# Kernel optimization log

Measured on AMD Instinct MI355X. Metric: run time of the kernel, lower is better.

## Reference

```python
import jax, jax.numpy as jnp
import numpy as np

LEAKY_SLOPE = 0.2

def setup_inputs() -> dict:
    key = jax.random.key(0)
    k1, k2, k3, k4, k5 = jax.random.split(key, 5)
    N, F_IN, H, D = 8192, 256, 4, 64
    x = jax.random.normal(k1, (N, F_IN), dtype=jnp.float32)
    adj = jax.random.randint(k2, (N, N), 0, 2, dtype=jnp.int32)
    W = jax.random.normal(k3, (F_IN, H * D), dtype=jnp.float32) * 0.05
    a_l = jax.random.normal(k4, (H, D), dtype=jnp.float32) * 0.05
    a_r = jax.random.normal(k5, (H, D), dtype=jnp.float32) * 0.05
    return {"x": x, "adj": adj, "W": W, "a_l": a_l, "a_r": a_r}

def reference(x, adj, W, a_l, a_r):
    N = x.shape[0]
    H, D = a_l.shape
    # projected node features: (N, H, D)
    h = (x @ W).reshape(N, H, D)
    score_l = jnp.einsum('nhd,hd->nh', h, a_l)  # (N, H)
    score_r = jnp.einsum('nhd,hd->nh', h, a_r)  # (N, H)
    # logits[i, j, h] = score_l[i, h] + score_r[j, h]
    logits = score_l[:, None, :] + score_r[None, :, :]
    logits = jax.nn.leaky_relu(logits, negative_slope=LEAKY_SLOPE)
    # mask: keep edge (i,j) if adj[i,j] + eye[i,j] != 0
    keep = (adj + jnp.eye(N, dtype=adj.dtype)) != 0  # (N, N)
    logits = jnp.where(keep[:, :, None], logits, -jnp.inf)
    # softmax over neighbors j (axis=1), matching torch softmax(dim=1)
    attn = jax.nn.softmax(logits, axis=1)  # (N, N, H)
    out = jnp.einsum('ijh,jhf->ihf', attn, h)  # (N, H, D)
    return out.reshape(N, H * D)  # concat=True
```

## Files before the change

### kernel.cpp

```cpp
#include <hip/hip_runtime.h>
#include <hip/hip_bf16.h>
#include <hip/hip_fp16.h>

#define N 8192
#define FIN 256
#define HD 256
#define LEAKY 0.2f

typedef short sh8 __attribute__((ext_vector_type(8)));
typedef _Float16 h8 __attribute__((ext_vector_type(8)));
typedef _Float16 h2 __attribute__((ext_vector_type(2)));
typedef float f32x4 __attribute__((ext_vector_type(4)));
typedef int   i32x4 __attribute__((ext_vector_type(4)));

__device__ __forceinline__ int pack2bf(float a, float b){
  __hip_bfloat162 t = __float22bfloat162_rn(make_float2(a, b));
  union { __hip_bfloat162 h; int i; } u;
  u.h = t;
  return u.i;
}

__device__ __forceinline__ h2 u2h2(unsigned u){ union{unsigned u; h2 h;} c; c.u=u; return c.h; }
__device__ __forceinline__ unsigned h22u(h2 h){ union{unsigned u; h2 h;} c; c.h=h; return c.u; }

__global__ void k_wt(const float* __restrict__ W, __hip_bfloat16* __restrict__ Wt){
  __shared__ float t[16][17];
  int tx = threadIdx.x, ty = threadIdx.y;
  int bx = blockIdx.x*16, by = blockIdx.y*16;
  t[ty][tx] = W[(by+ty)*HD + (bx+tx)];
  __syncthreads();
  Wt[(bx+ty)*FIN + (by+tx)] = __float2bfloat16(t[tx][ty]);
}

__global__ __launch_bounds__(256) void k_pack(const int* __restrict__ adj,
                                              unsigned* __restrict__ bits){
  const int g = blockIdx.x*256 + threadIdx.x;
  const i32x4 a = *(const i32x4*)(adj + (size_t)g*4);
  const int sub = g & 7;
  unsigned wpart = 0;
  #pragma unroll
  for (int e = 0; e < 4; ++e){
    const int jj = sub*4 + e;
    wpart |= ((unsigned)a[e] & 1u) << ((jj >> 1) + ((jj & 1) << 4));
  }
  wpart |= __shfl_xor(wpart, 1);
  wpart |= __shfl_xor(wpart, 2);
  wpart |= __shfl_xor(wpart, 4);
  if (sub == 0){
    const int t = g >> 3;
    const int i = t >> 8;
    const int c = t & 255;
    if ((i >> 5) == c){
      const int k = i & 31;
      wpart |= 1u << ((k >> 1) + ((k & 1) << 4));
    }
    bits[t] = wpart;
  }
}

__global__ __launch_bounds__(256, 2) void k_h(
    const float* __restrict__ x, const __hip_bfloat16* __restrict__ Wt,
    const float* __restrict__ a_l, const float* __restrict__ a_r,
    _Float16* __restrict__ ht, float* __restrict__ El, float* __restrict__ El2,
    _Float16* __restrict__ Erh, _Float16* __restrict__ Er2h)
{
  const int lane = threadIdx.x & 63;
  const int w = threadIdx.x >> 6;
  const int r0 = lane & 15, q = lane >> 4;
  const int c0 = w*64;
  const int n0 = blockIdx.x*16;

  f32x4 acc[4];
  #pragma unroll
  for (int m = 0; m < 4; ++m) acc[m] = (f32x4){0.f, 0.f, 0.f, 0.f};

  for (int kb = 0; kb < 8; ++kb){
    const int k = kb*32 + q*8;
    sh8 af[4];
    #pragma unroll
    for (int m = 0; m < 4; ++m)
      af[m] = *(const sh8*)(Wt + (c0 + m*16 + r0)*FIN + k);
    const float* xp = x + (n0 + r0)*FIN + k;
    f32x4 xl = *(const f32x4*)xp;
    f32x4 xh = *(const f32x4*)(xp + 4);
    union { sh8 s; int i[4]; } bx;
    bx.i[0] = pack2bf(xl[0], xl[1]);
    bx.i[1] = pack2bf(xl[2], xl[3]);
    bx.i[2] = pack2bf(xh[0], xh[1]);
    bx.i[3] = pack2bf(xh[2], xh[3]);
    #pragma unroll
    for (int m = 0; m < 4; ++m)
      acc[m] = __builtin_amdgcn_mfma_f32_16x16x32_bf16(af[m], bx.s, acc[m], 0, 0, 0);
  }

  float pl = 0.f, pr = 0.f;
  #pragma unroll
  for (int m = 0; m < 4; ++m){
    #pragma unroll
    for (int reg = 0; reg < 4; ++reg){
      const int c = c0 + m*16 + q*4 + reg;
      const float v = acc[m][reg];
      ht[(size_t)c*N + (n0 + r0)] = (_Float16)v;
      pl += v*a_l[c];
      pr += v*a_r[c];
    }
  }
  pl += __shfl_xor(pl, 16); pl += __shfl_xor(pl, 32);
  pr += __shfl_xor(pr, 16); pr += __shfl_xor(pr, 32);
  if (lane < 16){
    const int n = n0 + r0;
    El  [w*N + n] = __expf(pl);
    El2 [w*N + n] = __expf(LEAKY*pl);
    Erh [w*N + n] = (_Float16)__expf(pr);
    Er2h[w*N + n] = (_Float16)__expf(LEAKY*pr);
  }
}

__global__ __launch_bounds__(256, 4) void k_attn(
    const unsigned* __restrict__ bits, const _Float16* __restrict__ ht,
    const float* __restrict__ El, const float* __restrict__ El2,
    const _Float16* __restrict__ Erh, const _Float16* __restrict__ Er2h,
    float* __restrict__ part, float* __restrict__ zpart)
{
  __shared__ __align__(16) char smem[40960];
  const int b = blockIdx.x;
  const int h = b >> 8, jq = (b >> 6) & 3, i128 = b & 63;
  const int tid = threadIdx.x;
  const int lane = tid & 63;
  const int w = tid >> 6;
  const int r0 = lane & 15, q = lane >> 4;
  const int ib = i128*128 + w*32;
  const int jbase = jq * 2048;

  const _Float16* gp = ht + (size_t)(h*64 + w*16 + (lane >> 2))*N
                          + jbase + (((lane & 3) ^ ((lane >> 3) & 3))*8);
  char* lb = smem + w*1024;
  const char* frp = smem + r0*64 + ((q ^ ((r0 >> 1) & 3)) << 4);

  {
    const _Float16* s1 = Erh  + h*N + jbase + w*512 + lane*8;
    const _Float16* s2 = Er2h + h*N + jbase + w*512 + lane*8;
    __builtin_amdgcn_global_load_lds(
      (const __attribute__((address_space(1))) void*)s1,
      (__attribute__((address_space(3))) void*)(smem + 32768 + w*1024), 16, 0, 0);
    __builtin_amdgcn_global_load_lds(
      (const __attribute__((address_space(1))) void*)s2,
      (__attribute__((address_space(3))) void*)(smem + 36864 + w*1024), 16, 0, 0);
  }
  const char* erp1 = smem + 32768 + q*16;
  const char* erp2 = smem + 36864 + q*16;

  const float* el_ = El  + h*N + ib + r0;
  const float* el2_= El2 + h*N + ib + r0;
  h2 elh[2], el2h[2];
  #pragma unroll
  for (int m = 0; m < 2; ++m){
    _Float16 a = (_Float16)el_[m*16];
    _Float16 c = (_Float16)el2_[m*16];
    elh[m]  = (h2){a, a};
    el2h[m] = (h2){c, c};
  }

  const unsigned* bp0 = bits + (size_t)(ib + r0)*(N/32) + jq*64;
  const unsigned* bp1 = bp0 + 16*(N/32);
  const int qs = q*4;

  union { h8 s; int i[4]; } onef;
  {
    int v = (r0 == 0) ? 0x3C003C00 : 0;
    onef.i[0]=v; onef.i[1]=v; onef.i[2]=v; onef.i[3]=v;
  }

  f32x4 acc[2][4];
  f32x4 accz[2];
  #pragma unroll
  for (int m = 0; m < 2; ++m){
    accz[m] = (f32x4){0.f,0.f,0.f,0.f};
    #pragma unroll
    for (int d = 0; d < 4; ++d)
      acc[m][d] = (f32x4){0.f,0.f,0.f,0.f};
  }

#define STAGE(bufoff, t) do { \
    const _Float16* _g = gp + (t)*128; \
    _Pragma("unroll") \
    for (int _s = 0; _s < 4; ++_s) \
      __builtin_amdgcn_global_load_lds( \
        (const __attribute__((address_space(1))) void*)(_g + _s*32), \
        (__attribute__((address_space(3))) void*)(lb + (bufoff) + _s*4096), 16, 0, 0); \
  } while(0)

  i32x4 bcur[2], bnxt[2];
  bcur[0] = *(const i32x4*)(bp0);
  bcur[1] = *(const i32x4*)(bp1);
  STAGE(0, 0);
  __syncthreads();

  for (int t = 0; t < 16; ++t){
    const int bo = (t & 1) ? 16384 : 0;
    const int bn = bo ^ 16384;
    const int tn = (t + 1) & 15;
    STAGE(bn, tn);
    bnxt[0] = *(const i32x4*)(bp0 + tn*4);
    bnxt[1] = *(const i32x4*)(bp1 + tn*4);

    #pragma unroll
    for (int ss = 0; ss < 4; ++ss){
      i32x4 er4  = *(const i32x4*)(erp1 + t*256 + ss*64);
      i32x4 er24 = *(const i32x4*)(erp2 + t*256 + ss*64);

      h8 hf[4];
      #pragma unroll
      for (int d = 0; d < 4; ++d)
        hf[d] = *(const h8*)(frp + bo + ss*4096 + d*1024);

      #pragma unroll
      for (int m = 0; m < 2; ++m){
        const unsigned wq = ((unsigned)bcur[m][ss]) >> qs;
        unsigned fu[4];
        #pragma unroll
        for (int p = 0; p < 4; ++p){
          const unsigned t32 = (wq >> p) & 0x10001u;
          const unsigned msk = t32 * 0xFFFFu;
          h2 w2 = __builtin_elementwise_max(elh[m]  * u2h2((unsigned)er4[p]),
                                            el2h[m] * u2h2((unsigned)er24[p]));
          fu[p] = h22u(w2) & msk;
        }
        union { h8 s; unsigned u[4]; } fa;
        fa.u[0]=fu[0]; fa.u[1]=fu[1]; fa.u[2]=fu[2]; fa.u[3]=fu[3];
        #pragma unroll
        for (int d = 0; d < 4; ++d)
          acc[m][d] = __builtin_amdgcn_mfma_f32_16x16x32_f16(fa.s, hf[d], acc[m][d], 0, 0, 0);
        accz[m] = __builtin_amdgcn_mfma_f32_16x16x32_f16(fa.s, onef.s, accz[m], 0, 0, 0);
      }
    }

    bcur[0] = bnxt[0]; bcur[1] = bnxt[1];
    __syncthreads();
  }

  if (r0 == 0){
    #pragma unroll
    for (int m = 0; m < 2; ++m)
      #pragma unroll
      for (int reg = 0; reg < 4; ++reg)
        zpart[(jq*4 + h)*N + ib + m*16 + q*4 + reg] = accz[m][reg];
  }

  float* pp = part + (size_t)jq*N*HD + h*64 + r0;
  #pragma unroll
  for (int m = 0; m < 2; ++m)
    #pragma unroll
    for (int d = 0; d < 4; ++d)
      #pragma unroll
      for (int reg = 0; reg < 4; ++reg)
        pp[(size_t)(ib + m*16 + q*4 + reg)*HD + d*16] = acc[m][d][reg];
#undef STAGE
}

__global__ void k_out(const float* __restrict__ part, const float* __restrict__ zpart,
                      float* __restrict__ out)
{
  const int t4 = (blockIdx.x*256 + threadIdx.x) * 4;
  const int i = t4 >> 8;
  const int h = (t4 & 255) >> 6;
  f32x4 a = *(const f32x4*)(part + t4);
  f32x4 bq = *(const f32x4*)(part + (size_t)N*HD + t4);
  f32x4 c = *(const f32x4*)(part + 2*(size_t)N*HD + t4);
  f32x4 d = *(const f32x4*)(part + 3*(size_t)N*HD + t4);
  float zz = zpart[h*N + i] + zpart[(4 + h)*N + i] + zpart[(8 + h)*N + i] + zpart[(12 + h)*N + i];
  f32x4 s = (a + bq + c + d) / zz;
  *(f32x4*)(out + t4) = s;
}

extern "C" void kernel_launch(void* const* d_in, const int* in_sizes, int n_in,
                              void* d_out, int out_size, void* d_ws, size_t ws_size,
                              hipStream_t stream) {
  const float* x   = (const float*)d_in[0];
  const int*   adj = (const int*)d_in[1];
  const float* W   = (const float*)d_in[2];
  const float* a_l = (const float*)d_in[3];
  const float* a_r = (const float*)d_in[4];
  float* out = (float*)d_out;

  char* ws = (char*)d_ws;
  __hip_bfloat16* Wt = (__hip_bfloat16*)ws;
  _Float16* ht   = (_Float16*)(ws + 131072);
  float*    El   = (float*)   (ws + 4325376);
  float*    El2  = (float*)   (ws + 4456448);
  _Float16* Erh  = (_Float16*)(ws + 4587520);
  _Float16* Er2h = (_Float16*)(ws + 4653056);
  float*    part = (float*)   (ws + 4718592);
  float*    zpart= (float*)   (ws + 38273024);
  unsigned* bits = (unsigned*)(ws + 38797312);

  k_wt  <<<dim3(16,16), dim3(16,16), 0, stream>>>(W, Wt);
  k_pack<<<N*N/4/256, 256, 0, stream>>>(adj, bits);
  k_h   <<<512, 256, 0, stream>>>(x, Wt, a_l, a_r, ht, El, El2, Erh, Er2h);
  k_attn<<<1024, 256, 0, stream>>>(bits, ht, El, El2, Erh, Er2h, part, zpart);
  k_out <<<N*HD/1024, 256, 0, stream>>>(part, zpart, out);
}
```

Baseline: 429.4 us.

## Split attention j-range into eighths with triple-buffered LDS staging

The attention kernel now splits the neighbour dimension into 8 chunks of 1024 instead of 4 of 2048, doubling the grid to 2048 blocks. Each tile is half as large, and LDS use drops so occupancy can rise to 5 blocks per SM. The staging moves from a double buffer with __syncthreads to a three-slot ring with explicit vmcnt waits and raw barriers, keeping two tiles in flight, and MFMA sections get raised wave priority. The cost is twice as many partial-sum buffers, which k_out must read and reduce, adding global memory traffic.

```diff
diff --git a/kernel.cpp b/kernel.cpp
--- a/kernel.cpp
+++ b/kernel.cpp
@@ -12,6 +12,7 @@
 typedef _Float16 h2 __attribute__((ext_vector_type(2)));
 typedef float f32x4 __attribute__((ext_vector_type(4)));
 typedef int   i32x4 __attribute__((ext_vector_type(4)));
+typedef int   i32x2 __attribute__((ext_vector_type(2)));
 
 __device__ __forceinline__ int pack2bf(float a, float b){
   __hip_bfloat162 t = __float22bfloat162_rn(make_float2(a, b));
@@ -116,21 +117,21 @@
   }
 }
 
-__global__ __launch_bounds__(256, 4) void k_attn(
+__global__ __launch_bounds__(256, 5) void k_attn(
     const unsigned* __restrict__ bits, const _Float16* __restrict__ ht,
     const float* __restrict__ El, const float* __restrict__ El2,
     const _Float16* __restrict__ Erh, const _Float16* __restrict__ Er2h,
     float* __restrict__ part, float* __restrict__ zpart)
 {
-  __shared__ __align__(16) char smem[40960];
+  __shared__ __align__(16) char smem[28672];
   const int b = blockIdx.x;
-  const int h = b >> 8, jq = (b >> 6) & 3, i128 = b & 63;
+  const int h = b >> 9, jq = (b >> 6) & 7, i128 = b & 63;
   const int tid = threadIdx.x;
   const int lane = tid & 63;
   const int w = tid >> 6;
   const int r0 = lane & 15, q = lane >> 4;
   const int ib = i128*128 + w*32;
-  const int jbase = jq * 2048;
+  const int jbase = jq * 1024;
 
   const _Float16* gp = ht + (size_t)(h*64 + w*16 + (lane >> 2))*N
                           + jbase + (((lane & 3) ^ ((lane >> 3) & 3))*8);
@@ -138,17 +139,15 @@
   const char* frp = smem + r0*64 + ((q ^ ((r0 >> 1) & 3)) << 4);
 
   {
-    const _Float16* s1 = Erh  + h*N + jbase + w*512 + lane*8;
-    const _Float16* s2 = Er2h + h*N + jbase + w*512 + lane*8;
+    const int arr = w >> 1, half = w & 1;
+    const _Float16* src = (arr ? Er2h : Erh) + h*N + jbase + half*512 + lane*8;
     __builtin_amdgcn_global_load_lds(
-      (const __attribute__((address_space(1))) void*)s1,
-      (__attribute__((address_space(3))) void*)(smem + 32768 + w*1024), 16, 0, 0);
-    __builtin_amdgcn_global_load_lds(
-      (const __attribute__((address_space(1))) void*)s2,
-      (__attribute__((address_space(3))) void*)(smem + 36864 + w*1024), 16, 0, 0);
-  }
-  const char* erp1 = smem + 32768 + q*16;
-  const char* erp2 = smem + 36864 + q*16;
+      (const __attribute__((address_space(1))) void*)src,
+      (__attribute__((address_space(3))) void*)(smem + 24576 + arr*2048 + half*1024 + lane*16),
+      16, 0, 0);
+  }
+  const char* erp1 = smem + 24576 + q*16;
+  const char* erp2 = smem + 26624 + q*16;
 
   const float* el_ = El  + h*N + ib + r0;
   const float* el2_= El2 + h*N + ib + r0;
@@ -161,7 +160,7 @@
     el2h[m] = (h2){c, c};
   }
 
-  const unsigned* bp0 = bits + (size_t)(ib + r0)*(N/32) + jq*64;
+  const unsigned* bp0 = bits + (size_t)(ib + r0)*(N/32) + jq*32;
   const unsigned* bp1 = bp0 + 16*(N/32);
   const int qs = q*4;
 
@@ -182,41 +181,43 @@
   }
 
 #define STAGE(bufoff, t) do { \
-    const _Float16* _g = gp + (t)*128; \
+    const _Float16* _g = gp + (t)*64; \
     _Pragma("unroll") \
-    for (int _s = 0; _s < 4; ++_s) \
+    for (int _s = 0; _s < 2; ++_s) \
       __builtin_amdgcn_global_load_lds( \
         (const __attribute__((address_space(1))) void*)(_g + _s*32), \
         (__attribute__((address_space(3))) void*)(lb + (bufoff) + _s*4096), 16, 0, 0); \
   } while(0)
 
-  i32x4 bcur[2], bnxt[2];
-  bcur[0] = *(const i32x4*)(bp0);
-  bcur[1] = *(const i32x4*)(bp1);
+  i32x2 bc0, bc1, bn0, bn1;
+  bc0 = *(const i32x2*)(bp0);
+  bc1 = *(const i32x2*)(bp1);
   STAGE(0, 0);
-  __syncthreads();
-
+  STAGE(8192, 1);
+  asm volatile("s_waitcnt vmcnt(2)" ::: "memory");
+  __builtin_amdgcn_s_barrier();
+  __builtin_amdgcn_sched_barrier(0);
+
+  int br = 0, bs = 16384;
   for (int t = 0; t < 16; ++t){
-    const int bo = (t & 1) ? 16384 : 0;
-    const int bn = bo ^ 16384;
     const int tn = (t + 1) & 15;
-    STAGE(bn, tn);
-    bnxt[0] = *(const i32x4*)(bp0 + tn*4);
-    bnxt[1] = *(const i32x4*)(bp1 + tn*4);
-
-    #pragma unroll
-    for (int ss = 0; ss < 4; ++ss){
-      i32x4 er4  = *(const i32x4*)(erp1 + t*256 + ss*64);
-      i32x4 er24 = *(const i32x4*)(erp2 + t*256 + ss*64);
+    bn0 = *(const i32x2*)(bp0 + tn*2);
+    bn1 = *(const i32x2*)(bp1 + tn*2);
+    STAGE(bs, (t + 2) & 15);
+
+    #pragma unroll
+    for (int ss = 0; ss < 2; ++ss){
+      i32x4 er4  = *(const i32x4*)(erp1 + t*128 + ss*64);
+      i32x4 er24 = *(const i32x4*)(erp2 + t*128 + ss*64);
 
       h8 hf[4];
       #pragma unroll
       for (int d = 0; d < 4; ++d)
-        hf[d] = *(const h8*)(frp + bo + ss*4096 + d*1024);
+        hf[d] = *(const h8*)(frp + br + ss*4096 + d*1024);
 
       #pragma unroll
       for (int m = 0; m < 2; ++m){
-        const unsigned wq = ((unsigned)bcur[m][ss]) >> qs;
+        const unsigned wq = ((unsigned)(m ? bc1[ss] : bc0[ss])) >> qs;
         unsigned fu[4];
         #pragma unroll
         for (int p = 0; p < 4; ++p){
@@ -228,15 +229,21 @@
         }
         union { h8 s; unsigned u[4]; } fa;
         fa.u[0]=fu[0]; fa.u[1]=fu[1]; fa.u[2]=fu[2]; fa.u[3]=fu[3];
+        __builtin_amdgcn_s_setprio(1);
         #pragma unroll
         for (int d = 0; d < 4; ++d)
           acc[m][d] = __builtin_amdgcn_mfma_f32_16x16x32_f16(fa.s, hf[d], acc[m][d], 0, 0, 0);
         accz[m] = __builtin_amdgcn_mfma_f32_16x16x32_f16(fa.s, onef.s, accz[m], 0, 0, 0);
+        __builtin_amdgcn_s_setprio(0);
       }
     }
 
-    bcur[0] = bnxt[0]; bcur[1] = bnxt[1];
-    __syncthreads();
+    bc0 = bn0; bc1 = bn1;
+    br = (br == 16384) ? 0 : br + 8192;
+    bs = (bs == 16384) ? 0 : bs + 8192;
+    asm volatile("s_waitcnt vmcnt(4)" ::: "memory");
+    __builtin_amdgcn_s_barrier();
+    __builtin_amdgcn_sched_barrier(0);
   }
 
   if (r0 == 0){
@@ -264,12 +271,14 @@
   const int t4 = (blockIdx.x*256 + threadIdx.x) * 4;
   const int i = t4 >> 8;
   const int h = (t4 & 255) >> 6;
-  f32x4 a = *(const f32x4*)(part + t4);
-  f32x4 bq = *(const f32x4*)(part + (size_t)N*HD + t4);
-  f32x4 c = *(const f32x4*)(part + 2*(size_t)N*HD + t4);
-  f32x4 d = *(const f32x4*)(part + 3*(size_t)N*HD + t4);
-  float zz = zpart[h*N + i] + zpart[(4 + h)*N + i] + zpart[(8 + h)*N + i] + zpart[(12 + h)*N + i];
-  f32x4 s = (a + bq + c + d) / zz;
+  f32x4 s = (f32x4){0.f,0.f,0.f,0.f};
+  float zz = 0.f;
+  #pragma unroll
+  for (int jq = 0; jq < 8; ++jq){
+    s += *(const f32x4*)(part + (size_t)jq*N*HD + t4);
+    zz += zpart[(jq*4 + h)*N + i];
+  }
+  s = s / zz;
   *(f32x4*)(out + t4) = s;
 }
 
@@ -291,12 +300,12 @@
   _Float16* Erh  = (_Float16*)(ws + 4587520);
   _Float16* Er2h = (_Float16*)(ws + 4653056);
   float*    part = (float*)   (ws + 4718592);
-  float*    zpart= (float*)   (ws + 38273024);
-  unsigned* bits = (unsigned*)(ws + 38797312);
+  float*    zpart= (float*)   (ws + 71827456);
+  unsigned* bits = (unsigned*)(ws + 72876032);
 
   k_wt  <<<dim3(16,16), dim3(16,16), 0, stream>>>(W, Wt);
   k_pack<<<N*N/4/256, 256, 0, stream>>>(adj, bits);
   k_h   <<<512, 256, 0, stream>>>(x, Wt, a_l, a_r, ht, El, El2, Erh, Er2h);
-  k_attn<<<1024, 256, 0, stream>>>(bits, ht, El, El2, Erh, Er2h, part, zpart);
+  k_attn<<<2048, 256, 0, stream>>>(bits, ht, El, El2, Erh, Er2h, part, zpart);
   k_out <<<N*HD/1024, 256, 0, stream>>>(part, zpart, out);
 }
```

Measured after the change: 445.4 us. 3.7% more time.

## Load attention value fragments directly from global into registers, dropping LDS staging

Applied to the files above, without the earlier changes.

Value (ht) fragments are no longer staged cooperatively into a double-buffered LDS tile. Each lane now loads its MFMA B-operand fragments straight from global memory into registers, with a two-step register double buffer, and the per-tile block barriers are removed. LDS shrinks to 8KB, which holds only the exponentiated right scores, and s_setprio is wrapped around the MFMA groups. This removes the LDS round-trip and the syncs, but each wave now fetches its own copy of ht with no sharing across waves. The per-lane 16-byte loads are strided by rows of N and rely on L2 for reuse.

```diff
diff --git a/kernel.cpp b/kernel.cpp
--- a/kernel.cpp
+++ b/kernel.cpp
@@ -12,6 +12,7 @@
 typedef _Float16 h2 __attribute__((ext_vector_type(2)));
 typedef float f32x4 __attribute__((ext_vector_type(4)));
 typedef int   i32x4 __attribute__((ext_vector_type(4)));
+typedef int   i32x2 __attribute__((ext_vector_type(2)));
 
 __device__ __forceinline__ int pack2bf(float a, float b){
   __hip_bfloat162 t = __float22bfloat162_rn(make_float2(a, b));
@@ -122,7 +123,7 @@
     const _Float16* __restrict__ Erh, const _Float16* __restrict__ Er2h,
     float* __restrict__ part, float* __restrict__ zpart)
 {
-  __shared__ __align__(16) char smem[40960];
+  __shared__ __align__(16) char smem[8192];
   const int b = blockIdx.x;
   const int h = b >> 8, jq = (b >> 6) & 3, i128 = b & 63;
   const int tid = threadIdx.x;
@@ -132,23 +133,18 @@
   const int ib = i128*128 + w*32;
   const int jbase = jq * 2048;
 
-  const _Float16* gp = ht + (size_t)(h*64 + w*16 + (lane >> 2))*N
-                          + jbase + (((lane & 3) ^ ((lane >> 3) & 3))*8);
-  char* lb = smem + w*1024;
-  const char* frp = smem + r0*64 + ((q ^ ((r0 >> 1) & 3)) << 4);
-
   {
     const _Float16* s1 = Erh  + h*N + jbase + w*512 + lane*8;
     const _Float16* s2 = Er2h + h*N + jbase + w*512 + lane*8;
     __builtin_amdgcn_global_load_lds(
       (const __attribute__((address_space(1))) void*)s1,
-      (__attribute__((address_space(3))) void*)(smem + 32768 + w*1024), 16, 0, 0);
+      (__attribute__((address_space(3))) void*)(smem + w*1024), 16, 0, 0);
     __builtin_amdgcn_global_load_lds(
       (const __attribute__((address_space(1))) void*)s2,
-      (__attribute__((address_space(3))) void*)(smem + 36864 + w*1024), 16, 0, 0);
-  }
-  const char* erp1 = smem + 32768 + q*16;
-  const char* erp2 = smem + 36864 + q*16;
+      (__attribute__((address_space(3))) void*)(smem + 4096 + w*1024), 16, 0, 0);
+  }
+  const char* erp1 = smem + q*16;
+  const char* erp2 = smem + 4096 + q*16;
 
   const float* el_ = El  + h*N + ib + r0;
   const float* el2_= El2 + h*N + ib + r0;
@@ -161,6 +157,8 @@
     el2h[m] = (h2){c, c};
   }
 
+  const _Float16* hp = ht + (size_t)(h*64 + r0)*N + jbase + q*8;
+
   const unsigned* bp0 = bits + (size_t)(ib + r0)*(N/32) + jq*64;
   const unsigned* bp1 = bp0 + 16*(N/32);
   const int qs = q*4;
@@ -181,62 +179,57 @@
       acc[m][d] = (f32x4){0.f,0.f,0.f,0.f};
   }
 
-#define STAGE(bufoff, t) do { \
-    const _Float16* _g = gp + (t)*128; \
+#define PREF(buf, stp) do { \
+    const _Float16* _p = hp + (size_t)(stp)*32; \
+    buf[0] = *(const h8*)(_p); \
+    buf[1] = *(const h8*)(_p + (size_t)16*N); \
+    buf[2] = *(const h8*)(_p + (size_t)32*N); \
+    buf[3] = *(const h8*)(_p + (size_t)48*N); \
+  } while(0)
+
+#define STEPC(buf, stp, wrd0, wrd1) do { \
+    i32x4 er4  = *(const i32x4*)(erp1 + (stp)*64); \
+    i32x4 er24 = *(const i32x4*)(erp2 + (stp)*64); \
     _Pragma("unroll") \
-    for (int _s = 0; _s < 4; ++_s) \
-      __builtin_amdgcn_global_load_lds( \
-        (const __attribute__((address_space(1))) void*)(_g + _s*32), \
-        (__attribute__((address_space(3))) void*)(lb + (bufoff) + _s*4096), 16, 0, 0); \
+    for (int m = 0; m < 2; ++m){ \
+      const unsigned wq = ((m) ? (unsigned)(wrd1) : (unsigned)(wrd0)) >> qs; \
+      unsigned fu[4]; \
+      _Pragma("unroll") \
+      for (int p = 0; p < 4; ++p){ \
+        const unsigned t32 = (wq >> p) & 0x10001u; \
+        const unsigned msk = t32 * 0xFFFFu; \
+        h2 w2 = __builtin_elementwise_max(elh[m]  * u2h2((unsigned)er4[p]), \
+                                          el2h[m] * u2h2((unsigned)er24[p])); \
+        fu[p] = h22u(w2) & msk; \
+      } \
+      union { h8 s8; unsigned u[4]; } fa; \
+      fa.u[0]=fu[0]; fa.u[1]=fu[1]; fa.u[2]=fu[2]; fa.u[3]=fu[3]; \
+      __builtin_amdgcn_s_setprio(1); \
+      _Pragma("unroll") \
+      for (int d = 0; d < 4; ++d) \
+        acc[m][d] = __builtin_amdgcn_mfma_f32_16x16x32_f16(fa.s8, buf[d], acc[m][d], 0, 0, 0); \
+      accz[m] = __builtin_amdgcn_mfma_f32_16x16x32_f16(fa.s8, onef.s, accz[m], 0, 0, 0); \
+      __builtin_amdgcn_s_setprio(0); \
+    } \
   } while(0)
 
-  i32x4 bcur[2], bnxt[2];
-  bcur[0] = *(const i32x4*)(bp0);
-  bcur[1] = *(const i32x4*)(bp1);
-  STAGE(0, 0);
+  h8 A[4], B[4];
+  i32x2 bc0 = *(const i32x2*)bp0;
+  i32x2 bc1 = *(const i32x2*)bp1;
+  i32x2 bn0, bn1;
+  PREF(A, 0);
   __syncthreads();
 
-  for (int t = 0; t < 16; ++t){
-    const int bo = (t & 1) ? 16384 : 0;
-    const int bn = bo ^ 16384;
-    const int tn = (t + 1) & 15;
-    STAGE(bn, tn);
-    bnxt[0] = *(const i32x4*)(bp0 + tn*4);
-    bnxt[1] = *(const i32x4*)(bp1 + tn*4);
-
-    #pragma unroll
-    for (int ss = 0; ss < 4; ++ss){
-      i32x4 er4  = *(const i32x4*)(erp1 + t*256 + ss*64);
-      i32x4 er24 = *(const i32x4*)(erp2 + t*256 + ss*64);
-
-      h8 hf[4];
-      #pragma unroll
-      for (int d = 0; d < 4; ++d)
-        hf[d] = *(const h8*)(frp + bo + ss*4096 + d*1024);
-
-      #pragma unroll
-      for (int m = 0; m < 2; ++m){
-        const unsigned wq = ((unsigned)bcur[m][ss]) >> qs;
-        unsigned fu[4];
-        #pragma unroll
-        for (int p = 0; p < 4; ++p){
-          const unsigned t32 = (wq >> p) & 0x10001u;
-          const unsigned msk = t32 * 0xFFFFu;
-          h2 w2 = __builtin_elementwise_max(elh[m]  * u2h2((unsigned)er4[p]),
-                                            el2h[m] * u2h2((unsigned)er24[p]));
-          fu[p] = h22u(w2) & msk;
-        }
-        union { h8 s; unsigned u[4]; } fa;
-        fa.u[0]=fu[0]; fa.u[1]=fu[1]; fa.u[2]=fu[2]; fa.u[3]=fu[3];
-        #pragma unroll
-        for (int d = 0; d < 4; ++d)
-          acc[m][d] = __builtin_amdgcn_mfma_f32_16x16x32_f16(fa.s, hf[d], acc[m][d], 0, 0, 0);
-        accz[m] = __builtin_amdgcn_mfma_f32_16x16x32_f16(fa.s, onef.s, accz[m], 0, 0, 0);
-      }
-    }
-
-    bcur[0] = bnxt[0]; bcur[1] = bnxt[1];
-    __syncthreads();
+  for (int sp = 0; sp < 32; ++sp){
+    const int sB = sp*2 + 1;
+    const int spn = (sp + 1) & 31;
+    bn0 = *(const i32x2*)(bp0 + spn*2);
+    bn1 = *(const i32x2*)(bp1 + spn*2);
+    PREF(B, sB);
+    STEPC(A, sp*2, bc0[0], bc1[0]);
+    PREF(A, (sB + 1) & 63);
+    STEPC(B, sB, bc0[1], bc1[1]);
+    bc0 = bn0; bc1 = bn1;
   }
 
   if (r0 == 0){
@@ -255,7 +248,8 @@
       #pragma unroll
       for (int reg = 0; reg < 4; ++reg)
         pp[(size_t)(ib + m*16 + q*4 + reg)*HD + d*16] = acc[m][d][reg];
-#undef STAGE
+#undef PREF
+#undef STEPC
 }
 
 __global__ void k_out(const float* __restrict__ part, const float* __restrict__ zpart,
```

Result: slower. 526.7 us (+22.7%).
